# Kernel tuning notes

Measured on AMD Instinct MI355X. Metric: run time of the kernel, lower is better.

## Reference

```python
import jax, jax.numpy as jnp
import numpy as np

N = 100000      # nodes
E = 1600000     # edges (avg degree 16)
G = 64          # graphs in batch
IN_DIM, HID, C2, C3, HEADS, NCLS = 64, 128, 64, 32, 4, 5
EPS = 1e-5
NEG_SLOPE = 0.2


def setup_inputs() -> dict:
    key = jax.random.key(0)
    ks = jax.random.split(key, 32)

    def w(k, fan_in, shape):
        return jax.random.normal(k, shape, dtype=jnp.float32) * (1.0 / np.sqrt(fan_in))

    x = jax.random.normal(ks[0], (N, IN_DIM), dtype=jnp.float32)
    edge_index = jax.random.randint(ks[1], (2, E), 0, N)
    batch = jnp.sort(jax.random.randint(ks[2], (N,), 0, G))

    inp = {"x": x, "edge_index": edge_index, "batch": batch}
    # GCN layers (PyG GCNConv: weight then symmetric-normalized aggregation, bias after)
    inp.update(W1=w(ks[3], IN_DIM, (IN_DIM, HID)), b1=jnp.zeros((HID,), jnp.float32))
    inp.update(W2=w(ks[4], HID, (HID, C2)), b2=jnp.zeros((C2,), jnp.float32))
    inp.update(W3=w(ks[5], C2, (C2, C3)), b3=jnp.zeros((C3,), jnp.float32))
    # BatchNorm (inference: running stats)
    def bn_params(k, d):
        k1, k2, k3 = jax.random.split(k, 3)
        return (1.0 + 0.1 * jax.random.normal(k1, (d,), jnp.float32),
                0.1 * jax.random.normal(k2, (d,), jnp.float32),
                0.1 * jax.random.normal(k3, (d,), jnp.float32),
                jax.random.uniform(k, (d,), jnp.float32, 0.5, 1.5))
    inp["g1"], inp["be1"], inp["m1"], inp["v1"] = bn_params(ks[6], HID)
    inp["g2"], inp["be2"], inp["m2"], inp["v2"] = bn_params(ks[7], C2)
    inp["g3"], inp["be3"], inp["m3"], inp["v3"] = bn_params(ks[8], C3)
    # GAT (heads=4, out=32, concat=False -> mean over heads)
    inp["Wg"] = w(ks[9], C3, (C3, HEADS * C3))
    inp["ag_s"] = w(ks[10], C3, (HEADS, C3))
    inp["ag_d"] = w(ks[11], C3, (HEADS, C3))
    inp["bg"] = jnp.zeros((C3,), jnp.float32)
    # classifier MLP 32 -> 16 -> 5
    inp["Wc1"] = w(ks[12], C3, (C3, 16)); inp["bc1"] = jnp.zeros((16,), jnp.float32)
    inp["Wc2"] = w(ks[13], 16, (16, NCLS)); inp["bc2"] = jnp.zeros((NCLS,), jnp.float32)
    return inp


def _bn(h, g, be, m, v):
    return (h - m) * jax.lax.rsqrt(v + EPS) * g + be


def reference(x, edge_index, batch,
              W1, b1, g1, be1, m1, v1,
              W2, b2, g2, be2, m2, v2,
              W3, b3, g3, be3, m3, v3,
              Wg, ag_s, ag_d, bg,
              Wc1, bc1, Wc2, bc2):
    n = x.shape[0]
    loop = jnp.arange(n)
    src = jnp.concatenate([edge_index[0], loop])  # add self-loops (PyG default)
    dst = jnp.concatenate([edge_index[1], loop])

    # GCN symmetric normalization: deg from dst (col), norm = d^-1/2[src]*d^-1/2[dst]
    deg = jnp.zeros((n,), x.dtype).at[dst].add(1.0)
    dinv = jax.lax.rsqrt(deg)  # deg >= 1 due to self-loops
    norm = (dinv[src] * dinv[dst])[:, None]

    def gcn(h, W, b):
        h = h @ W
        return jax.ops.segment_sum(h[src] * norm, dst, num_segments=n) + b

    h = jax.nn.relu(_bn(gcn(x, W1, b1), g1, be1, m1, v1))
    h = jax.nn.relu(_bn(gcn(h, W2, b2), g2, be2, m2, v2))
    h = jax.nn.relu(_bn(gcn(h, W3, b3), g3, be3, m3, v3))

    # GAT: per-edge attention, segment softmax over incoming edges per dst
    hh = (h @ Wg).reshape(n, HEADS, C3)          # [N,H,D]
    a_s = jnp.einsum('nhd,hd->nh', hh, ag_s)     # [N,H]
    a_d = jnp.einsum('nhd,hd->nh', hh, ag_d)
    e = jax.nn.leaky_relu(a_s[src] + a_d[dst], NEG_SLOPE)  # [Eall,H]
    emax = jax.lax.stop_gradient(jax.ops.segment_max(e, dst, num_segments=n))
    ee = jnp.exp(e - emax[dst])
    den = jax.ops.segment_sum(ee, dst, num_segments=n)
    att = ee / den[dst]                          # [Eall,H]
    agg = jax.ops.segment_sum(att[:, :, None] * hh[src], dst, num_segments=n)
    h = jax.nn.relu(agg.mean(axis=1) + bg)       # concat=False -> mean heads

    # global mean pool over graphs
    cnt = jax.ops.segment_sum(jnp.ones((n,), h.dtype), batch, num_segments=G)
    pooled = jax.ops.segment_sum(h, batch, num_segments=G) / jnp.maximum(cnt, 1.0)[:, None]

    # classifier (dropout inactive in eval)
    out = jax.nn.relu(pooled @ Wc1 + bc1) @ Wc2 + bc2
    return out
```

## Files before the change

### kernel.cpp

```cpp
#include <hip/hip_runtime.h>

#define EPSN   1e-5f
#define NEGS   0.2f
#define NGRAPH 64
#define BSHIFT 9
#define NPBK   512
#define GCAP   96

__device__ __forceinline__ float lrelu(float e) { return e > 0.f ? e : NEGS * e; }

__global__ void k_bin_count(const int* __restrict__ ed, int* __restrict__ bsize,
                            int E, int NB) {
    __shared__ int lcnt[1024];
    for (int i = threadIdx.x; i < NB; i += 256) lcnt[i] = 0;
    __syncthreads();
    int chunk = (E + gridDim.x - 1) / gridDim.x;
    int lo = blockIdx.x * chunk;
    int hi = min(E, lo + chunk);
    for (int e = lo + threadIdx.x; e < hi; e += 256)
        atomicAdd(&lcnt[ed[e] >> BSHIFT], 1);
    __syncthreads();
    for (int b = threadIdx.x; b < NB; b += 256)
        if (lcnt[b]) atomicAdd(&bsize[b], lcnt[b]);
}
__global__ void k_bucket_scan(const int* __restrict__ bsize, int* __restrict__ bbase,
                              int* __restrict__ gcur, int NB) {
    int lane = threadIdx.x;
    if (lane >= 64) return;
    int carry = 0;
    int rounds = (NB + 63) / 64;
    for (int r = 0; r < rounds; ++r) {
        int idx = r * 64 + lane;
        int orig = (idx < NB) ? bsize[idx] : 0;
        int v = orig;
#pragma unroll
        for (int o = 1; o < 64; o <<= 1) {
            int t = __shfl_up(v, o, 64);
            if (lane >= o) v += t;
        }
        if (idx < NB) {
            int excl = carry + v - orig;
            bbase[idx] = excl;
            gcur[idx] = excl;
        }
        carry += __shfl(v, 63, 64);
    }
}
__global__ void k_bin_write(const int* __restrict__ es, const int* __restrict__ ed,
                            int* __restrict__ gcur, int2* __restrict__ binned,
                            int E, int NB) {
    __shared__ int lcnt[1024];
    __shared__ int lofs[1024];
    int chunk = (E + gridDim.x - 1) / gridDim.x;
    int lo = blockIdx.x * chunk;
    int hi = min(E, lo + chunk);
    for (int i = threadIdx.x; i < NB; i += 256) lcnt[i] = 0;
    __syncthreads();
    for (int e = lo + threadIdx.x; e < hi; e += 256)
        atomicAdd(&lcnt[ed[e] >> BSHIFT], 1);
    __syncthreads();
    for (int b = threadIdx.x; b < NB; b += 256) {
        int c = lcnt[b];
        lofs[b] = c ? atomicAdd(&gcur[b], c) : 0;
    }
    __syncthreads();
    for (int i = threadIdx.x; i < NB; i += 256) lcnt[i] = 0;
    __syncthreads();
    for (int e = lo + threadIdx.x; e < hi; e += 256) {
        int s = es[e], t = ed[e];
        int b = t >> BSHIFT;
        int pos = lofs[b] + atomicAdd(&lcnt[b], 1);
        binned[pos] = make_int2(s, t);
    }
}
__global__ void k_csr_build(const int2* __restrict__ binned, const int* __restrict__ bbase,
                            const int* __restrict__ bsize, int* __restrict__ rowptr,
                            int* __restrict__ deg, float* __restrict__ dinv,
                            int* __restrict__ csrc, int N) {
    __shared__ int cnt_l[NPBK];
    __shared__ int ofs_l[NPBK];
    int b = blockIdx.x;
    int base = bbase[b];
    int cnt = bsize[b];
    int nlo = b << BSHIFT;
    int nhi = min(N, nlo + NPBK);
    int nv = nhi - nlo;
    int csrbase = base + nlo;
    int tid = threadIdx.x;
    for (int i = tid; i < NPBK; i += 256) cnt_l[i] = (i < nv) ? 1 : 0;
    __syncthreads();
    for (int e = tid; e < cnt; e += 256) {
        int2 st = binned[base + e];
        atomicAdd(&cnt_l[st.y - nlo], 1);
    }
    __syncthreads();
    if (tid < 64) {
        int carry = 0;
#pragma unroll
        for (int r = 0; r < NPBK / 64; ++r) {
            int idx = r * 64 + tid;
            int orig = cnt_l[idx];
            int v = orig;
#pragma unroll
            for (int o = 1; o < 64; o <<= 1) {
                int t = __shfl_up(v, o, 64);
                if (tid >= o) v += t;
            }
            ofs_l[idx] = carry + v - orig;
            carry += __shfl(v, 63, 64);
        }
    }
    __syncthreads();
    for (int i = tid; i < nv; i += 256) {
        int node = nlo + i;
        int d = cnt_l[i];
        rowptr[node] = csrbase + ofs_l[i];
        deg[node] = d;
        dinv[node] = rsqrtf((float)d);
    }
    __syncthreads();
    for (int i = tid; i < NPBK; i += 256) cnt_l[i] = ofs_l[i];
    __syncthreads();
    for (int e = tid; e < cnt; e += 256) {
        int2 st = binned[base + e];
        int p = atomicAdd(&cnt_l[st.y - nlo], 1);
        csrc[csrbase + p] = st.x;
    }
    for (int i = tid; i < nv; i += 256) {
        int p = atomicAdd(&cnt_l[i], 1);
        csrc[csrbase + p] = nlo + i;
    }
}

template <int K, int M, int EPI>
__global__ void k_matmul4(const float* __restrict__ X, const float* __restrict__ W,
                          float* __restrict__ Y, int n,
                          const float* __restrict__ b, const float* __restrict__ g,
                          const float* __restrict__ be, const float* __restrict__ m,
                          const float* __restrict__ v, const float* __restrict__ dinv) {
    __shared__ float Wl[K * M];
    for (int i = threadIdx.x; i < K * M / 4; i += 256)
        ((float4*)Wl)[i] = ((const float4*)W)[i];
    __syncthreads();
    const int TPR = M / 4;
    const int RPB = 256 / TPR;
    const int c4  = (threadIdx.x % TPR) * 4;
    int row = blockIdx.x * RPB + threadIdx.x / TPR;
    if (row >= n) return;
    const float4* xr = (const float4*)(X + (long long)row * K);
    float4 acc = make_float4(0.f, 0.f, 0.f, 0.f);
#pragma unroll
    for (int k4 = 0; k4 < K / 4; ++k4) {
        float4 xv = xr[k4];
        const float* wp = &Wl[(k4 * 4) * M + c4];
        float4 w0 = *(const float4*)(wp);
        float4 w1 = *(const float4*)(wp + M);
        float4 w2 = *(const float4*)(wp + 2 * M);
        float4 w3 = *(const float4*)(wp + 3 * M);
        acc.x += xv.x * w0.x + xv.y * w1.x + xv.z * w2.x + xv.w * w3.x;
        acc.y += xv.x * w0.y + xv.y * w1.y + xv.z * w2.y + xv.w * w3.y;
        acc.z += xv.x * w0.z + xv.y * w1.z + xv.z * w2.z + xv.w * w3.z;
        acc.w += xv.x * w0.w + xv.y * w1.w + xv.z * w2.w + xv.w * w3.w;
    }
    if (EPI == 1) {
        float4 bb = *(const float4*)(b + c4);
        float4 mm = *(const float4*)(m + c4);
        float4 vv = *(const float4*)(v + c4);
        float4 gg = *(const float4*)(g + c4);
        float4 ee = *(const float4*)(be + c4);
        acc.x = fmaxf((acc.x + bb.x - mm.x) * rsqrtf(vv.x + EPSN) * gg.x + ee.x, 0.f);
        acc.y = fmaxf((acc.y + bb.y - mm.y) * rsqrtf(vv.y + EPSN) * gg.y + ee.y, 0.f);
        acc.z = fmaxf((acc.z + bb.z - mm.z) * rsqrtf(vv.z + EPSN) * gg.z + ee.z, 0.f);
        acc.w = fmaxf((acc.w + bb.w - mm.w) * rsqrtf(vv.w + EPSN) * gg.w + ee.w, 0.f);
    } else if (EPI == 2) {
        float din = dinv[row];
        acc.x *= din; acc.y *= din; acc.z *= din; acc.w *= din;
    }
    *(float4*)(Y + (long long)row * M + c4) = acc;
}

template <int M, int EPI, int PRE>
__global__ void k_agg4(const float* __restrict__ A, const int* __restrict__ rowptr,
                       const int* __restrict__ deg, const int* __restrict__ csrc,
                       const float* __restrict__ dinv,
                       const float* __restrict__ b, const float* __restrict__ g,
                       const float* __restrict__ be, const float* __restrict__ m,
                       const float* __restrict__ v,
                       float* __restrict__ B, int n) {
    const int LPE = M / 4;
    const int EPW = 64 / LPE;
    int node = blockIdx.x * 4 + (threadIdx.x >> 6);
    if (node >= n) return;
    int lane = threadIdx.x & 63;
    int eg = lane / LPE;
    int dl = lane % LPE;
    int beg = rowptr[node];
    int end = beg + deg[node];
    float4 acc = make_float4(0.f, 0.f, 0.f, 0.f);
    int i = beg + eg;
    for (; i + EPW < end; i += 2 * EPW) {
        int s0 = csrc[i];
        int s1 = csrc[i + EPW];
        float4 x0 = *(const float4*)(A + (long long)s0 * M + dl * 4);
        float4 x1 = *(const float4*)(A + (long long)s1 * M + dl * 4);
        if (PRE) {
            float w0 = dinv[s0], w1 = dinv[s1];
            x0.x *= w0; x0.y *= w0; x0.z *= w0; x0.w *= w0;
            x1.x *= w1; x1.y *= w1; x1.z *= w1; x1.w *= w1;
        }
        acc.x += x0.x + x1.x; acc.y += x0.y + x1.y;
        acc.z += x0.z + x1.z; acc.w += x0.w + x1.w;
    }
    if (i < end) {
        int s = csrc[i];
        float4 xv = *(const float4*)(A + (long long)s * M + dl * 4);
        if (PRE) {
            float w0 = dinv[s];
            xv.x *= w0; xv.y *= w0; xv.z *= w0; xv.w *= w0;
        }
        acc.x += xv.x; acc.y += xv.y; acc.z += xv.z; acc.w += xv.w;
    }
#pragma unroll
    for (int off = LPE; off < 64; off <<= 1) {
        acc.x += __shfl_xor(acc.x, off);
        acc.y += __shfl_xor(acc.y, off);
        acc.z += __shfl_xor(acc.z, off);
        acc.w += __shfl_xor(acc.w, off);
    }
    if (eg == 0) {
        float din = dinv[node];
        acc.x *= din; acc.y *= din; acc.z *= din; acc.w *= din;
        if (EPI == 1) {
            int d0 = dl * 4;
            float4 bb = *(const float4*)(b + d0);
            float4 mm = *(const float4*)(m + d0);
            float4 vv = *(const float4*)(v + d0);
            float4 gg = *(const float4*)(g + d0);
            float4 ee = *(const float4*)(be + d0);
            acc.x = fmaxf((acc.x + bb.x - mm.x) * rsqrtf(vv.x + EPSN) * gg.x + ee.x, 0.f);
            acc.y = fmaxf((acc.y + bb.y - mm.y) * rsqrtf(vv.y + EPSN) * gg.y + ee.y, 0.f);
            acc.z = fmaxf((acc.z + bb.z - mm.z) * rsqrtf(vv.z + EPSN) * gg.z + ee.z, 0.f);
            acc.w = fmaxf((acc.w + bb.w - mm.w) * rsqrtf(vv.w + EPSN) * gg.w + ee.w, 0.f);
        }
        *(float4*)(B + (long long)node * M + dl * 4) = acc;
    }
}

__global__ void k_wsd(const float* __restrict__ Wg, const float* __restrict__ ags,
                      const float* __restrict__ agd, float* __restrict__ wsd) {
    int j = threadIdx.x;
    if (j < 128) {
        int k = j >> 2, h = j & 3;
        float ss = 0.f, dd = 0.f;
        for (int d2 = 0; d2 < 32; ++d2) {
            float wv = Wg[k * 128 + h * 32 + d2];
            ss += wv * ags[h * 32 + d2];
            dd += wv * agd[h * 32 + d2];
        }
        wsd[j] = ss;
        wsd[128 + j] = dd;
    }
}

__global__ void k_agg_att(const float* __restrict__ A, const int* __restrict__ rowptr,
                          const int* __restrict__ deg, const int* __restrict__ csrc,
                          const float* __restrict__ dinv,
                          const float* __restrict__ b, const float* __restrict__ g,
                          const float* __restrict__ be, const float* __restrict__ m,
                          const float* __restrict__ v, const float* __restrict__ wsd,
                          float* __restrict__ H3, float* __restrict__ a_s,
                          float* __restrict__ a_d, int n) {
    __shared__ float Wl[256];
    for (int i = threadIdx.x; i < 256; i += 256) Wl[i] = wsd[i];
    __syncthreads();
    const int M = 32, LPE = 8, EPW = 8;
    int node = blockIdx.x * 4 + (threadIdx.x >> 6);
    if (node >= n) return;
    int lane = threadIdx.x & 63;
    int eg = lane >> 3;
    int dl = lane & 7;
    int beg = rowptr[node];
    int end = beg + deg[node];
    float4 acc = make_float4(0.f, 0.f, 0.f, 0.f);
    int i = beg + eg;
    for (; i + EPW < end; i += 2 * EPW) {
        int s0 = csrc[i];
        int s1 = csrc[i + EPW];
        float4 x0 = *(const float4*)(A + (long long)s0 * M + dl * 4);
        float4 x1 = *(const float4*)(A + (long long)s1 * M + dl * 4);
        acc.x += x0.x + x1.x; acc.y += x0.y + x1.y;
        acc.z += x0.z + x1.z; acc.w += x0.w + x1.w;
    }
    if (i < end) {
        int s = csrc[i];
        float4 xv = *(const float4*)(A + (long long)s * M + dl * 4);
        acc.x += xv.x; acc.y += xv.y; acc.z += xv.z; acc.w += xv.w;
    }
#pragma unroll
    for (int off = 8; off < 64; off <<= 1) {
        acc.x += __shfl_xor(acc.x, off);
        acc.y += __shfl_xor(acc.y, off);
        acc.z += __shfl_xor(acc.z, off);
        acc.w += __shfl_xor(acc.w, off);
    }
    float din = dinv[node];
    int d0 = dl * 4;
    float4 bb = *(const float4*)(b + d0);
    float4 mm = *(const float4*)(m + d0);
    float4 vv = *(const float4*)(v + d0);
    float4 gg = *(const float4*)(g + d0);
    float4 ee = *(const float4*)(be + d0);
    float4 hv;
    hv.x = fmaxf((acc.x * din + bb.x - mm.x) * rsqrtf(vv.x + EPSN) * gg.x + ee.x, 0.f);
    hv.y = fmaxf((acc.y * din + bb.y - mm.y) * rsqrtf(vv.y + EPSN) * gg.y + ee.y, 0.f);
    hv.z = fmaxf((acc.z * din + bb.z - mm.z) * rsqrtf(vv.z + EPSN) * gg.z + ee.z, 0.f);
    hv.w = fmaxf((acc.w * din + bb.w - mm.w) * rsqrtf(vv.w + EPSN) * gg.w + ee.w, 0.f);
    if (eg == 0)
        *(float4*)(H3 + (long long)node * M + d0) = hv;
    int h = lane & 3, sel = (lane >> 2) & 1;
    const float* wp = &Wl[sel * 128];
    float o = 0.f;
#pragma unroll
    for (int src = 0; src < 8; ++src) {
        float bx = __shfl(hv.x, src);
        float by = __shfl(hv.y, src);
        float bz = __shfl(hv.z, src);
        float bw = __shfl(hv.w, src);
        int k0 = src * 4;
        o += bx * wp[k0 * 4 + h] + by * wp[(k0 + 1) * 4 + h] +
             bz * wp[(k0 + 2) * 4 + h] + bw * wp[(k0 + 3) * 4 + h];
    }
    if (lane < 4) a_s[node * 4 + h] = o;
    else if (lane < 8) a_d[node * 4 + h] = o;
}

__global__ void k_gat4(const float* __restrict__ H3, const float* __restrict__ a_s,
                       const float* __restrict__ a_d, const int* __restrict__ rowptr,
                       const int* __restrict__ deg, const int* __restrict__ csrc,
                       const float* __restrict__ Wg, const float* __restrict__ bg,
                       float* __restrict__ H4, int n) {
    __shared__ float sc[4][GCAP * 4];
    __shared__ int   srcb[4][GCAP];
    __shared__ float wb[4][128];
    int w = threadIdx.x >> 6;
    int node = blockIdx.x * 4 + w;
    if (node >= n) return;
    int lane = threadIdx.x & 63;
    int beg = rowptr[node];
    int cnt = deg[node];
    bool fits = (cnt <= GCAP);
    float4 ad4 = ((const float4*)a_d)[node];
    float m0 = -1e30f, m1 = -1e30f, m2 = -1e30f, m3 = -1e30f;
    if (fits) {
        for (int e = lane; e < cnt; e += 64) {
            int s = csrc[beg + e];
            srcb[w][e] = s;
            float4 as = ((const float4*)a_s)[s];
            float e0 = lrelu(as.x + ad4.x);
            float e1 = lrelu(as.y + ad4.y);
            float e2 = lrelu(as.z + ad4.z);
            float e3 = lrelu(as.w + ad4.w);
            *(float4*)&sc[w][e * 4] = make_float4(e0, e1, e2, e3);
            m0 = fmaxf(m0, e0); m1 = fmaxf(m1, e1);
            m2 = fmaxf(m2, e2); m3 = fmaxf(m3, e3);
        }
    } else {
        for (int e = lane; e < cnt; e += 64) {
            int s = csrc[beg + e];
            float4 as = ((const float4*)a_s)[s];
            m0 = fmaxf(m0, lrelu(as.x + ad4.x));
            m1 = fmaxf(m1, lrelu(as.y + ad4.y));
            m2 = fmaxf(m2, lrelu(as.z + ad4.z));
            m3 = fmaxf(m3, lrelu(as.w + ad4.w));
        }
    }
#pragma unroll
    for (int o = 1; o < 64; o <<= 1) {
        m0 = fmaxf(m0, __shfl_xor(m0, o));
        m1 = fmaxf(m1, __shfl_xor(m1, o));
        m2 = fmaxf(m2, __shfl_xor(m2, o));
        m3 = fmaxf(m3, __shfl_xor(m3, o));
    }
    float s0 = 0.f, s1 = 0.f, s2 = 0.f, s3 = 0.f;
    if (fits) {
        for (int e = lane; e < cnt; e += 64) {
            float4 sv = *(float4*)&sc[w][e * 4];
            float p0 = __expf(sv.x - m0);
            float p1 = __expf(sv.y - m1);
            float p2 = __expf(sv.z - m2);
            float p3 = __expf(sv.w - m3);
            *(float4*)&sc[w][e * 4] = make_float4(p0, p1, p2, p3);
            s0 += p0; s1 += p1; s2 += p2; s3 += p3;
        }
    } else {
        for (int e = lane; e < cnt; e += 64) {
            int s = csrc[beg + e];
            float4 as = ((const float4*)a_s)[s];
            s0 += __expf(lrelu(as.x + ad4.x) - m0);
            s1 += __expf(lrelu(as.y + ad4.y) - m1);
            s2 += __expf(lrelu(as.z + ad4.z) - m2);
            s3 += __expf(lrelu(as.w + ad4.w) - m3);
        }
    }
#pragma unroll
    for (int o = 1; o < 64; o <<= 1) {
        s0 += __shfl_xor(s0, o);
        s1 += __shfl_xor(s1, o);
        s2 += __shfl_xor(s2, o);
        s3 += __shfl_xor(s3, o);
    }
    float inv0 = 0.25f / s0, inv1 = 0.25f / s1, inv2 = 0.25f / s2, inv3 = 0.25f / s3;
    int d = lane & 31;
    int h0 = lane >> 5;
    float invA = (h0 == 0) ? inv0 : inv1;
    float invB = (h0 == 0) ? inv2 : inv3;
    float a0 = 0.f, a1 = 0.f;
    if (fits) {
        int i = 0;
        for (; i + 4 <= cnt; i += 4) {
            int sA = srcb[w][i],     sB = srcb[w][i + 1];
            int sC = srcb[w][i + 2], sD = srcb[w][i + 3];
            float x0 = H3[(long long)sA * 32 + d];
            float x1 = H3[(long long)sB * 32 + d];
            float x2 = H3[(long long)sC * 32 + d];
            float x3 = H3[(long long)sD * 32 + d];
            float wA0 = sc[w][i * 4 + h0],       wA1 = sc[w][i * 4 + h0 + 2];
            float wB0 = sc[w][(i + 1) * 4 + h0], wB1 = sc[w][(i + 1) * 4 + h0 + 2];
            float wC0 = sc[w][(i + 2) * 4 + h0], wC1 = sc[w][(i + 2) * 4 + h0 + 2];
            float wD0 = sc[w][(i + 3) * 4 + h0], wD1 = sc[w][(i + 3) * 4 + h0 + 2];
            a0 += wA0 * x0 + wB0 * x1 + wC0 * x2 + wD0 * x3;
            a1 += wA1 * x0 + wB1 * x1 + wC1 * x2 + wD1 * x3;
        }
        for (; i < cnt; ++i) {
            int s = srcb[w][i];
            float x = H3[(long long)s * 32 + d];
            a0 += sc[w][i * 4 + h0] * x;
            a1 += sc[w][i * 4 + h0 + 2] * x;
        }
        a0 *= invA; a1 *= invB;
    } else {
        float mA = (h0 == 0) ? m0 : m1;
        float mB = (h0 == 0) ? m2 : m3;
        float adA = (h0 == 0) ? ad4.x : ad4.y;
        float adB = (h0 == 0) ? ad4.z : ad4.w;
        for (int i = 0; i < cnt; ++i) {
            int s = csrc[beg + i];
            float4 as = ((const float4*)a_s)[s];
            float eA = (h0 == 0) ? (as.x + adA) : (as.y + adA);
            float eB = (h0 == 0) ? (as.z + adB) : (as.w + adB);
            float x = H3[(long long)s * 32 + d];
            a0 += __expf(lrelu(eA) - mA) * x;
            a1 += __expf(lrelu(eB) - mB) * x;
        }
        a0 *= invA; a1 *= invB;
    }
    wb[w][lane] = a0;
    wb[w][64 + lane] = a1;
    int half = h0 * 64;
    float o = 0.f;
#pragma unroll
    for (int j = 0; j < 64; ++j) {
        int jj = half + j;
        o += wb[w][jj] * Wg[(jj & 31) * 128 + (jj >> 5) * 32 + d];
    }
    o += __shfl_xor(o, 32);
    if (lane < 32)
        H4[(long long)node * 32 + d] = fmaxf(o + bg[d], 0.f);
}

__global__ void k_pool_init(float* __restrict__ pooled, float* __restrict__ cnt) {
    int i = blockIdx.x * blockDim.x + threadIdx.x;
    if (i < NGRAPH * 32) pooled[i] = 0.f;
    if (i < NGRAPH) cnt[i] = 0.f;
}
__global__ void k_pool2(const float* __restrict__ h, const int* __restrict__ batch,
                        float* __restrict__ pooled, float* __restrict__ cnt, int n) {
    __shared__ float lp[NGRAPH * 32];
    __shared__ float lc[NGRAPH];
    int tid = threadIdx.x;
    for (int i = tid; i < NGRAPH * 32; i += 256) lp[i] = 0.f;
    for (int i = tid; i < NGRAPH; i += 256) lc[i] = 0.f;
    __syncthreads();
    int per = (n + gridDim.x - 1) / gridDim.x;
    int lo = blockIdx.x * per;
    int hi = min(n, lo + per);
    for (long long i = (long long)lo * 32 + tid; i < (long long)hi * 32; i += 256) {
        int ni = (int)(i >> 5), dd = (int)(i & 31);
        int b = batch[ni];
        atomicAdd(&lp[b * 32 + dd], h[i]);
        if (dd == 0) atomicAdd(&lc[b], 1.f);
    }
    __syncthreads();
    for (int i = tid; i < NGRAPH * 32; i += 256)
        if (lp[i] != 0.f) atomicAdd(&pooled[i], lp[i]);
    for (int i = tid; i < NGRAPH; i += 256)
        if (lc[i] != 0.f) atomicAdd(&cnt[i], lc[i]);
}

__global__ void k_classifier(const float* __restrict__ pooled, const float* __restrict__ cnt,
                             const float* __restrict__ Wc1, const float* __restrict__ bc1,
                             const float* __restrict__ Wc2, const float* __restrict__ bc2,
                             float* __restrict__ out) {
    __shared__ float pl[NGRAPH * 32];
    __shared__ float t1[NGRAPH * 16];
    int tid = threadIdx.x;
    for (int i = tid; i < NGRAPH * 32; i += blockDim.x) {
        int g = i >> 5;
        pl[i] = pooled[i] / fmaxf(cnt[g], 1.f);
    }
    __syncthreads();
    for (int i = tid; i < NGRAPH * 16; i += blockDim.x) {
        int g = i >> 4, c = i & 15;
        float acc = bc1[c];
#pragma unroll
        for (int d = 0; d < 32; ++d) acc += pl[g * 32 + d] * Wc1[d * 16 + c];
        t1[i] = fmaxf(acc, 0.f);
    }
    __syncthreads();
    for (int i = tid; i < NGRAPH * 5; i += blockDim.x) {
        int g = i / 5, c = i % 5;
        float acc = bc2[c];
#pragma unroll
        for (int k = 0; k < 16; ++k) acc += t1[g * 16 + k] * Wc2[k * 5 + c];
        out[i] = acc;
    }
}

static inline dim3 gsz(long long work, int block = 256) {
    long long g = (work + block - 1) / block;
    if (g > 262144) g = 262144;
    if (g < 1) g = 1;
    return dim3((unsigned)g);
}

extern "C" void kernel_launch(void* const* d_in, const int* in_sizes, int n_in,
                              void* d_out, int out_size, void* d_ws, size_t ws_size,
                              hipStream_t stream) {
    const float* x     = (const float*)d_in[0];
    const int*   ei    = (const int*)d_in[1];
    const int*   batch = (const int*)d_in[2];
    const float* W1 = (const float*)d_in[3];  const float* b1 = (const float*)d_in[4];
    const float* W2 = (const float*)d_in[5];  const float* b2 = (const float*)d_in[6];
    const float* W3 = (const float*)d_in[7];  const float* b3 = (const float*)d_in[8];
    const float* g1 = (const float*)d_in[9];  const float* be1 = (const float*)d_in[10];
    const float* m1 = (const float*)d_in[11]; const float* v1  = (const float*)d_in[12];
    const float* g2 = (const float*)d_in[13]; const float* be2 = (const float*)d_in[14];
    const float* m2 = (const float*)d_in[15]; const float* v2  = (const float*)d_in[16];
    const float* g3 = (const float*)d_in[17]; const float* be3 = (const float*)d_in[18];
    const float* m3 = (const float*)d_in[19]; const float* v3  = (const float*)d_in[20];
    const float* Wg  = (const float*)d_in[21];
    const float* ags = (const float*)d_in[22];
    const float* agd = (const float*)d_in[23];
    const float* bg  = (const float*)d_in[24];
    const float* Wc1 = (const float*)d_in[25]; const float* bc1 = (const float*)d_in[26];
    const float* Wc2 = (const float*)d_in[27]; const float* bc2 = (const float*)d_in[28];
    float* out = (float*)d_out;

    const int N = in_sizes[0] / 64;
    const int E = in_sizes[1] / 2;
    const int* esrc = ei;
    const int* edst = ei + E;
    const int NB = (N + NPBK - 1) >> BSHIFT;

    size_t off = 0;
    auto take = [&](size_t bytes) -> void* {
        void* p = (char*)d_ws + off;
        off += bytes;
        off = (off + 255) & ~(size_t)255;
        return p;
    };
    int*   deg    = (int*)take((size_t)N * 4);
    float* dinv   = (float*)take((size_t)N * 4);
    int*   rowptr = (int*)take((size_t)N * 4);
    int*   bsize  = (int*)take((size_t)1024 * 4);
    int*   bbase  = (int*)take((size_t)1024 * 4);
    int*   gcur   = (int*)take((size_t)1024 * 4);
    float* wsd    = (float*)take((size_t)256 * 4);
    int*   csrc   = (int*)take((size_t)(E + N) * 4);
    float* bufA   = (float*)take((size_t)N * 64 * 4);
    float* bufB   = (float*)take((size_t)N * 64 * 4);
    float* bufC   = (float*)take((size_t)N * 128 * 4);
    float* a_s    = (float*)take((size_t)N * 4 * 4);
    float* a_d    = (float*)take((size_t)N * 4 * 4);
    float* pooled = (float*)take((size_t)NGRAPH * 32 * 4);
    float* cnt    = (float*)take((size_t)NGRAPH * 4);
    int2*  binned = (int2*)bufC;
    (void)ws_size; (void)n_in; (void)out_size;

    const dim3 B256(256);
    const float* nil = nullptr;

    hipMemsetAsync(bsize, 0, (size_t)NB * 4, stream);
    hipLaunchKernelGGL(k_bin_count, dim3(512), B256, 0, stream, edst, bsize, E, NB);
    hipLaunchKernelGGL(k_bucket_scan, dim3(1), dim3(64), 0, stream, bsize, bbase, gcur, NB);
    hipLaunchKernelGGL(k_bin_write, dim3(512), B256, 0, stream, esrc, edst, gcur, binned, E, NB);
    hipLaunchKernelGGL(k_csr_build, dim3(NB), B256, 0, stream,
                       binned, bbase, bsize, rowptr, deg, dinv, csrc, N);
    hipLaunchKernelGGL(k_wsd, dim3(1), dim3(128), 0, stream, Wg, ags, agd, wsd);

    hipLaunchKernelGGL((k_agg4<64, 0, 1>), dim3((N + 3) / 4), B256, 0, stream,
                       x, rowptr, deg, csrc, dinv, nil, nil, nil, nil, nil, bufB, N);
    hipLaunchKernelGGL((k_matmul4<64, 128, 1>), dim3((N + 7) / 8), B256, 0, stream,
                       bufB, W1, bufC, N, b1, g1, be1, m1, v1, nil);
    hipLaunchKernelGGL((k_matmul4<128, 64, 2>), dim3((N + 15) / 16), B256, 0, stream,
                       bufC, W2, bufA, N, nil, nil, nil, nil, nil, dinv);
    hipLaunchKernelGGL((k_agg4<64, 1, 0>), dim3((N + 3) / 4), B256, 0, stream,
                       bufA, rowptr, deg, csrc, dinv, b2, g2, be2, m2, v2, bufB, N);
    hipLaunchKernelGGL((k_matmul4<64, 32, 2>), dim3((N + 31) / 32), B256, 0, stream,
                       bufB, W3, bufA, N, nil, nil, nil, nil, nil, dinv);
    hipLaunchKernelGGL(k_agg_att, dim3((N + 3) / 4), B256, 0, stream,
                       bufA, rowptr, deg, csrc, dinv, b3, g3, be3, m3, v3,
                       wsd, bufB, a_s, a_d, N);

    hipLaunchKernelGGL(k_gat4, dim3((N + 3) / 4), B256, 0, stream,
                       bufB, a_s, a_d, rowptr, deg, csrc, Wg, bg, bufA, N);

    hipLaunchKernelGGL(k_pool_init, dim3(9), B256, 0, stream, pooled, cnt);
    hipLaunchKernelGGL(k_pool2, dim3(128), B256, 0, stream, bufA, batch, pooled, cnt, N);
    hipLaunchKernelGGL(k_classifier, dim3(1), B256, 0, stream, pooled, cnt, Wc1, bc1, Wc2, bc2, out);
}
```

Before: 655.1 us.

## Store gathered node features in fp16 to halve neighbor gather bandwidth

Node feature buffers read by the edge aggregations (input x, the GCN layer-2 and layer-3 projected features, and the GAT input H3) are now stored as fp16. They are converted back to fp32 for accumulation. A new kernel pre-scales x by dinv and converts it to fp16, replacing the in-loop dinv multiply. The GAT aggregation is restructured so each lane loads half2 features and accumulates all four heads at once. This cuts memory traffic of the gather-bound aggregations, at the cost of reduced precision and an extra conversion pass.

Result: faster. 633.1 us (-3.4%).

```diff
diff --git a/kernel.cpp b/kernel.cpp
--- a/kernel.cpp
+++ b/kernel.cpp
@@ -6,6 +6,11 @@
 #define BSHIFT 9
 #define NPBK   512
 #define GCAP   96
+
+typedef _Float16 half_t;
+typedef _Float16 halfv8 __attribute__((ext_vector_type(8)));
+typedef _Float16 halfv4 __attribute__((ext_vector_type(4)));
+typedef _Float16 halfv2 __attribute__((ext_vector_type(2)));
 
 __device__ __forceinline__ float lrelu(float e) { return e > 0.f ? e : NEGS * e; }
 
@@ -132,12 +137,29 @@
     }
 }
 
-template <int K, int M, int EPI>
+__global__ void k_cvt_xh(const float* __restrict__ x, const float* __restrict__ dinv,
+                         half_t* __restrict__ xh, int n) {
+    int total = n * 8;
+    for (int q = blockIdx.x * blockDim.x + threadIdx.x; q < total;
+         q += gridDim.x * blockDim.x) {
+        float din = dinv[q >> 3];
+        float4 a = ((const float4*)x)[q * 2];
+        float4 b = ((const float4*)x)[q * 2 + 1];
+        halfv8 h;
+        h[0] = (half_t)(a.x * din); h[1] = (half_t)(a.y * din);
+        h[2] = (half_t)(a.z * din); h[3] = (half_t)(a.w * din);
+        h[4] = (half_t)(b.x * din); h[5] = (half_t)(b.y * din);
+        h[6] = (half_t)(b.z * din); h[7] = (half_t)(b.w * din);
+        ((halfv8*)xh)[q] = h;
+    }
+}
+
+template <int K, int M>
 __global__ void k_matmul4(const float* __restrict__ X, const float* __restrict__ W,
                           float* __restrict__ Y, int n,
                           const float* __restrict__ b, const float* __restrict__ g,
                           const float* __restrict__ be, const float* __restrict__ m,
-                          const float* __restrict__ v, const float* __restrict__ dinv) {
+                          const float* __restrict__ v) {
     __shared__ float Wl[K * M];
     for (int i = threadIdx.x; i < K * M / 4; i += 256)
         ((float4*)Wl)[i] = ((const float4*)W)[i];
@@ -162,32 +184,61 @@
         acc.z += xv.x * w0.z + xv.y * w1.z + xv.z * w2.z + xv.w * w3.z;
         acc.w += xv.x * w0.w + xv.y * w1.w + xv.z * w2.w + xv.w * w3.w;
     }
-    if (EPI == 1) {
-        float4 bb = *(const float4*)(b + c4);
-        float4 mm = *(const float4*)(m + c4);
-        float4 vv = *(const float4*)(v + c4);
-        float4 gg = *(const float4*)(g + c4);
-        float4 ee = *(const float4*)(be + c4);
-        acc.x = fmaxf((acc.x + bb.x - mm.x) * rsqrtf(vv.x + EPSN) * gg.x + ee.x, 0.f);
-        acc.y = fmaxf((acc.y + bb.y - mm.y) * rsqrtf(vv.y + EPSN) * gg.y + ee.y, 0.f);
-        acc.z = fmaxf((acc.z + bb.z - mm.z) * rsqrtf(vv.z + EPSN) * gg.z + ee.z, 0.f);
-        acc.w = fmaxf((acc.w + bb.w - mm.w) * rsqrtf(vv.w + EPSN) * gg.w + ee.w, 0.f);
-    } else if (EPI == 2) {
-        float din = dinv[row];
-        acc.x *= din; acc.y *= din; acc.z *= din; acc.w *= din;
-    }
+    float4 bb = *(const float4*)(b + c4);
+    float4 mm = *(const float4*)(m + c4);
+    float4 vv = *(const float4*)(v + c4);
+    float4 gg = *(const float4*)(g + c4);
+    float4 ee = *(const float4*)(be + c4);
+    acc.x = fmaxf((acc.x + bb.x - mm.x) * rsqrtf(vv.x + EPSN) * gg.x + ee.x, 0.f);
+    acc.y = fmaxf((acc.y + bb.y - mm.y) * rsqrtf(vv.y + EPSN) * gg.y + ee.y, 0.f);
+    acc.z = fmaxf((acc.z + bb.z - mm.z) * rsqrtf(vv.z + EPSN) * gg.z + ee.z, 0.f);
+    acc.w = fmaxf((acc.w + bb.w - mm.w) * rsqrtf(vv.w + EPSN) * gg.w + ee.w, 0.f);
     *(float4*)(Y + (long long)row * M + c4) = acc;
 }
 
-template <int M, int EPI, int PRE>
-__global__ void k_agg4(const float* __restrict__ A, const int* __restrict__ rowptr,
-                       const int* __restrict__ deg, const int* __restrict__ csrc,
-                       const float* __restrict__ dinv,
-                       const float* __restrict__ b, const float* __restrict__ g,
-                       const float* __restrict__ be, const float* __restrict__ m,
-                       const float* __restrict__ v,
-                       float* __restrict__ B, int n) {
-    const int LPE = M / 4;
+template <int K, int M>
+__global__ void k_matmul4h(const float* __restrict__ X, const float* __restrict__ W,
+                           half_t* __restrict__ Y, int n, const float* __restrict__ dinv) {
+    __shared__ float Wl[K * M];
+    for (int i = threadIdx.x; i < K * M / 4; i += 256)
+        ((float4*)Wl)[i] = ((const float4*)W)[i];
+    __syncthreads();
+    const int TPR = M / 4;
+    const int RPB = 256 / TPR;
+    const int c4  = (threadIdx.x % TPR) * 4;
+    int row = blockIdx.x * RPB + threadIdx.x / TPR;
+    if (row >= n) return;
+    const float4* xr = (const float4*)(X + (long long)row * K);
+    float4 acc = make_float4(0.f, 0.f, 0.f, 0.f);
+#pragma unroll
+    for (int k4 = 0; k4 < K / 4; ++k4) {
+        float4 xv = xr[k4];
+        const float* wp = &Wl[(k4 * 4) * M + c4];
+        float4 w0 = *(const float4*)(wp);
+        float4 w1 = *(const float4*)(wp + M);
+        float4 w2 = *(const float4*)(wp + 2 * M);
+        float4 w3 = *(const float4*)(wp + 3 * M);
+        acc.x += xv.x * w0.x + xv.y * w1.x + xv.z * w2.x + xv.w * w3.x;
+        acc.y += xv.x * w0.y + xv.y * w1.y + xv.z * w2.y + xv.w * w3.y;
+        acc.z += xv.x * w0.z + xv.y * w1.z + xv.z * w2.z + xv.w * w3.z;
+        acc.w += xv.x * w0.w + xv.y * w1.w + xv.z * w2.w + xv.w * w3.w;
+    }
+    float din = dinv[row];
+    halfv4 hv;
+    hv[0] = (half_t)(acc.x * din); hv[1] = (half_t)(acc.y * din);
+    hv[2] = (half_t)(acc.z * din); hv[3] = (half_t)(acc.w * din);
+    *(halfv4*)(Y + (long long)row * M + c4) = hv;
+}
+
+template <int M, int EPI>
+__global__ void k_agg4h(const half_t* __restrict__ A, const int* __restrict__ rowptr,
+                        const int* __restrict__ deg, const int* __restrict__ csrc,
+                        const float* __restrict__ dinv,
+                        const float* __restrict__ b, const float* __restrict__ g,
+                        const float* __restrict__ be, const float* __restrict__ m,
+                        const float* __restrict__ v,
+                        float* __restrict__ B, int n) {
+    const int LPE = M / 8;
     const int EPW = 64 / LPE;
     int node = blockIdx.x * 4 + (threadIdx.x >> 6);
     if (node >= n) return;
@@ -196,53 +247,46 @@
     int dl = lane % LPE;
     int beg = rowptr[node];
     int end = beg + deg[node];
-    float4 acc = make_float4(0.f, 0.f, 0.f, 0.f);
+    float acc[8];
+#pragma unroll
+    for (int j = 0; j < 8; ++j) acc[j] = 0.f;
     int i = beg + eg;
     for (; i + EPW < end; i += 2 * EPW) {
         int s0 = csrc[i];
         int s1 = csrc[i + EPW];
-        float4 x0 = *(const float4*)(A + (long long)s0 * M + dl * 4);
-        float4 x1 = *(const float4*)(A + (long long)s1 * M + dl * 4);
-        if (PRE) {
-            float w0 = dinv[s0], w1 = dinv[s1];
-            x0.x *= w0; x0.y *= w0; x0.z *= w0; x0.w *= w0;
-            x1.x *= w1; x1.y *= w1; x1.z *= w1; x1.w *= w1;
-        }
-        acc.x += x0.x + x1.x; acc.y += x0.y + x1.y;
-        acc.z += x0.z + x1.z; acc.w += x0.w + x1.w;
+        halfv8 x0 = *(const halfv8*)(A + (long long)s0 * M + dl * 8);
+        halfv8 x1 = *(const halfv8*)(A + (long long)s1 * M + dl * 8);
+#pragma unroll
+        for (int j = 0; j < 8; ++j) acc[j] += (float)x0[j] + (float)x1[j];
     }
     if (i < end) {
         int s = csrc[i];
-        float4 xv = *(const float4*)(A + (long long)s * M + dl * 4);
-        if (PRE) {
-            float w0 = dinv[s];
-            xv.x *= w0; xv.y *= w0; xv.z *= w0; xv.w *= w0;
-        }
-        acc.x += xv.x; acc.y += xv.y; acc.z += xv.z; acc.w += xv.w;
+        halfv8 xv = *(const halfv8*)(A + (long long)s * M + dl * 8);
+#pragma unroll
+        for (int j = 0; j < 8; ++j) acc[j] += (float)xv[j];
     }
 #pragma unroll
     for (int off = LPE; off < 64; off <<= 1) {
-        acc.x += __shfl_xor(acc.x, off);
-        acc.y += __shfl_xor(acc.y, off);
-        acc.z += __shfl_xor(acc.z, off);
-        acc.w += __shfl_xor(acc.w, off);
+#pragma unroll
+        for (int j = 0; j < 8; ++j) acc[j] += __shfl_xor(acc[j], off);
     }
     if (eg == 0) {
         float din = dinv[node];
-        acc.x *= din; acc.y *= din; acc.z *= din; acc.w *= din;
+        int d0 = dl * 8;
+        float o[8];
+#pragma unroll
+        for (int j = 0; j < 8; ++j) o[j] = acc[j] * din;
         if (EPI == 1) {
-            int d0 = dl * 4;
-            float4 bb = *(const float4*)(b + d0);
-            float4 mm = *(const float4*)(m + d0);
-            float4 vv = *(const float4*)(v + d0);
-            float4 gg = *(const float4*)(g + d0);
-            float4 ee = *(const float4*)(be + d0);
-            acc.x = fmaxf((acc.x + bb.x - mm.x) * rsqrtf(vv.x + EPSN) * gg.x + ee.x, 0.f);
-            acc.y = fmaxf((acc.y + bb.y - mm.y) * rsqrtf(vv.y + EPSN) * gg.y + ee.y, 0.f);
-            acc.z = fmaxf((acc.z + bb.z - mm.z) * rsqrtf(vv.z + EPSN) * gg.z + ee.z, 0.f);
-            acc.w = fmaxf((acc.w + bb.w - mm.w) * rsqrtf(vv.w + EPSN) * gg.w + ee.w, 0.f);
-        }
-        *(float4*)(B + (long long)node * M + dl * 4) = acc;
+#pragma unroll
+            for (int j = 0; j < 8; ++j) {
+                int d = d0 + j;
+                o[j] = fmaxf((o[j] + b[d] - m[d]) * rsqrtf(v[d] + EPSN) * g[d] + be[d], 0.f);
+            }
+        }
+        float4 lo = make_float4(o[0], o[1], o[2], o[3]);
+        float4 hi = make_float4(o[4], o[5], o[6], o[7]);
+        *(float4*)(B + (long long)node * M + d0) = lo;
+        *(float4*)(B + (long long)node * M + d0 + 4) = hi;
     }
 }
 
@@ -262,79 +306,78 @@
     }
 }
 
-__global__ void k_agg_att(const float* __restrict__ A, const int* __restrict__ rowptr,
+__global__ void k_agg_att(const half_t* __restrict__ A, const int* __restrict__ rowptr,
                           const int* __restrict__ deg, const int* __restrict__ csrc,
                           const float* __restrict__ dinv,
                           const float* __restrict__ b, const float* __restrict__ g,
                           const float* __restrict__ be, const float* __restrict__ m,
                           const float* __restrict__ v, const float* __restrict__ wsd,
-                          float* __restrict__ H3, float* __restrict__ a_s,
+                          half_t* __restrict__ H3h, float* __restrict__ a_s,
                           float* __restrict__ a_d, int n) {
     __shared__ float Wl[256];
     for (int i = threadIdx.x; i < 256; i += 256) Wl[i] = wsd[i];
     __syncthreads();
-    const int M = 32, LPE = 8, EPW = 8;
+    const int M = 32, LPE = 4, EPW = 16;
     int node = blockIdx.x * 4 + (threadIdx.x >> 6);
     if (node >= n) return;
     int lane = threadIdx.x & 63;
-    int eg = lane >> 3;
-    int dl = lane & 7;
+    int eg = lane >> 2;
+    int dl = lane & 3;
     int beg = rowptr[node];
     int end = beg + deg[node];
-    float4 acc = make_float4(0.f, 0.f, 0.f, 0.f);
+    float acc[8];
+#pragma unroll
+    for (int j = 0; j < 8; ++j) acc[j] = 0.f;
     int i = beg + eg;
     for (; i + EPW < end; i += 2 * EPW) {
         int s0 = csrc[i];
         int s1 = csrc[i + EPW];
-        float4 x0 = *(const float4*)(A + (long long)s0 * M + dl * 4);
-        float4 x1 = *(const float4*)(A + (long long)s1 * M + dl * 4);
-        acc.x += x0.x + x1.x; acc.y += x0.y + x1.y;
-        acc.z += x0.z + x1.z; acc.w += x0.w + x1.w;
+        halfv8 x0 = *(const halfv8*)(A + (long long)s0 * M + dl * 8);
+        halfv8 x1 = *(const halfv8*)(A + (long long)s1 * M + dl * 8);
+#pragma unroll
+        for (int j = 0; j < 8; ++j) acc[j] += (float)x0[j] + (float)x1[j];
     }
     if (i < end) {
         int s = csrc[i];
-        float4 xv = *(const float4*)(A + (long long)s * M + dl * 4);
-        acc.x += xv.x; acc.y += xv.y; acc.z += xv.z; acc.w += xv.w;
-    }
-#pragma unroll
-    for (int off = 8; off < 64; off <<= 1) {
-        acc.x += __shfl_xor(acc.x, off);
-        acc.y += __shfl_xor(acc.y, off);
-        acc.z += __shfl_xor(acc.z, off);
-        acc.w += __shfl_xor(acc.w, off);
+        halfv8 xv = *(const halfv8*)(A + (long long)s * M + dl * 8);
+#pragma unroll
+        for (int j = 0; j < 8; ++j) acc[j] += (float)xv[j];
+    }
+#pragma unroll
+    for (int off = 4; off < 64; off <<= 1) {
+#pragma unroll
+        for (int j = 0; j < 8; ++j) acc[j] += __shfl_xor(acc[j], off);
     }
     float din = dinv[node];
-    int d0 = dl * 4;
-    float4 bb = *(const float4*)(b + d0);
-    float4 mm = *(const float4*)(m + d0);
-    float4 vv = *(const float4*)(v + d0);
-    float4 gg = *(const float4*)(g + d0);
-    float4 ee = *(const float4*)(be + d0);
-    float4 hv;
-    hv.x = fmaxf((acc.x * din + bb.x - mm.x) * rsqrtf(vv.x + EPSN) * gg.x + ee.x, 0.f);
-    hv.y = fmaxf((acc.y * din + bb.y - mm.y) * rsqrtf(vv.y + EPSN) * gg.y + ee.y, 0.f);
-    hv.z = fmaxf((acc.z * din + bb.z - mm.z) * rsqrtf(vv.z + EPSN) * gg.z + ee.z, 0.f);
-    hv.w = fmaxf((acc.w * din + bb.w - mm.w) * rsqrtf(vv.w + EPSN) * gg.w + ee.w, 0.f);
-    if (eg == 0)
-        *(float4*)(H3 + (long long)node * M + d0) = hv;
+    int d0 = dl * 8;
+    float hv[8];
+#pragma unroll
+    for (int j = 0; j < 8; ++j) {
+        int d = d0 + j;
+        hv[j] = fmaxf((acc[j] * din + b[d] - m[d]) * rsqrtf(v[d] + EPSN) * g[d] + be[d], 0.f);
+    }
+    if (eg == 0) {
+        halfv8 hw;
+#pragma unroll
+        for (int j = 0; j < 8; ++j) hw[j] = (half_t)hv[j];
+        *(halfv8*)(H3h + (long long)node * M + d0) = hw;
+    }
     int h = lane & 3, sel = (lane >> 2) & 1;
     const float* wp = &Wl[sel * 128];
     float o = 0.f;
 #pragma unroll
-    for (int src = 0; src < 8; ++src) {
-        float bx = __shfl(hv.x, src);
-        float by = __shfl(hv.y, src);
-        float bz = __shfl(hv.z, src);
-        float bw = __shfl(hv.w, src);
-        int k0 = src * 4;
-        o += bx * wp[k0 * 4 + h] + by * wp[(k0 + 1) * 4 + h] +
-             bz * wp[(k0 + 2) * 4 + h] + bw * wp[(k0 + 3) * 4 + h];
+    for (int src = 0; src < 4; ++src) {
+#pragma unroll
+        for (int j = 0; j < 8; ++j) {
+            float xv = __shfl(hv[j], src);
+            o += xv * wp[(src * 8 + j) * 4 + h];
+        }
     }
     if (lane < 4) a_s[node * 4 + h] = o;
     else if (lane < 8) a_d[node * 4 + h] = o;
 }
 
-__global__ void k_gat4(const float* __restrict__ H3, const float* __restrict__ a_s,
+__global__ void k_gat4(const half_t* __restrict__ H3h, const float* __restrict__ a_s,
                        const float* __restrict__ a_d, const int* __restrict__ rowptr,
                        const int* __restrict__ deg, const int* __restrict__ csrc,
                        const float* __restrict__ Wg, const float* __restrict__ bg,
@@ -410,57 +453,73 @@
         s3 += __shfl_xor(s3, o);
     }
     float inv0 = 0.25f / s0, inv1 = 0.25f / s1, inv2 = 0.25f / s2, inv3 = 0.25f / s3;
+    int q = lane >> 4;
+    int k = lane & 15;
+    float acc[8];
+#pragma unroll
+    for (int j = 0; j < 8; ++j) acc[j] = 0.f;
+    if (fits) {
+        int i = q;
+        for (; i + 4 < cnt; i += 8) {
+            int sA = srcb[w][i];
+            int sB = srcb[w][i + 4];
+            halfv2 xA = *(const halfv2*)(H3h + (long long)sA * 32 + 2 * k);
+            halfv2 xB = *(const halfv2*)(H3h + (long long)sB * 32 + 2 * k);
+            float4 wA = *(float4*)&sc[w][i * 4];
+            float4 wB = *(float4*)&sc[w][(i + 4) * 4];
+            float a0 = (float)xA[0], a1 = (float)xA[1];
+            float b0 = (float)xB[0], b1 = (float)xB[1];
+            acc[0] += wA.x * a0 + wB.x * b0; acc[1] += wA.x * a1 + wB.x * b1;
+            acc[2] += wA.y * a0 + wB.y * b0; acc[3] += wA.y * a1 + wB.y * b1;
+            acc[4] += wA.z * a0 + wB.z * b0; acc[5] += wA.z * a1 + wB.z * b1;
+            acc[6] += wA.w * a0 + wB.w * b0; acc[7] += wA.w * a1 + wB.w * b1;
+        }
+        if (i < cnt) {
+            int s = srcb[w][i];
+            halfv2 xv = *(const halfv2*)(H3h + (long long)s * 32 + 2 * k);
+            float4 wv = *(float4*)&sc[w][i * 4];
+            float x0 = (float)xv[0], x1 = (float)xv[1];
+            acc[0] += wv.x * x0; acc[1] += wv.x * x1;
+            acc[2] += wv.y * x0; acc[3] += wv.y * x1;
+            acc[4] += wv.z * x0; acc[5] += wv.z * x1;
+            acc[6] += wv.w * x0; acc[7] += wv.w * x1;
+        }
+    } else {
+        for (int i = q; i < cnt; i += 4) {
+            int s = csrc[beg + i];
+            float4 as = ((const float4*)a_s)[s];
+            float p0 = __expf(lrelu(as.x + ad4.x) - m0);
+            float p1 = __expf(lrelu(as.y + ad4.y) - m1);
+            float p2 = __expf(lrelu(as.z + ad4.z) - m2);
+            float p3 = __expf(lrelu(as.w + ad4.w) - m3);
+            halfv2 xv = *(const halfv2*)(H3h + (long long)s * 32 + 2 * k);
+            float x0 = (float)xv[0], x1 = (float)xv[1];
+            acc[0] += p0 * x0; acc[1] += p0 * x1;
+            acc[2] += p1 * x0; acc[3] += p1 * x1;
+            acc[4] += p2 * x0; acc[5] += p2 * x1;
+            acc[6] += p3 * x0; acc[7] += p3 * x1;
+        }
+    }
+#pragma unroll
+    for (int o = 16; o < 64; o <<= 1) {
+#pragma unroll
+        for (int j = 0; j < 8; ++j) acc[j] += __shfl_xor(acc[j], o);
+    }
+    if (q == 0) {
+        float invh[4] = {inv0, inv1, inv2, inv3};
+#pragma unroll
+        for (int h = 0; h < 4; ++h) {
+            wb[w][h * 32 + 2 * k]     = acc[h * 2]     * invh[h];
+            wb[w][h * 32 + 2 * k + 1] = acc[h * 2 + 1] * invh[h];
+        }
+    }
     int d = lane & 31;
     int h0 = lane >> 5;
-    float invA = (h0 == 0) ? inv0 : inv1;
-    float invB = (h0 == 0) ? inv2 : inv3;
-    float a0 = 0.f, a1 = 0.f;
-    if (fits) {
-        int i = 0;
-        for (; i + 4 <= cnt; i += 4) {
-            int sA = srcb[w][i],     sB = srcb[w][i + 1];
-            int sC = srcb[w][i + 2], sD = srcb[w][i + 3];
-            float x0 = H3[(long long)sA * 32 + d];
-            float x1 = H3[(long long)sB * 32 + d];
-            float x2 = H3[(long long)sC * 32 + d];
-            float x3 = H3[(long long)sD * 32 + d];
-            float wA0 = sc[w][i * 4 + h0],       wA1 = sc[w][i * 4 + h0 + 2];
-            float wB0 = sc[w][(i + 1) * 4 + h0], wB1 = sc[w][(i + 1) * 4 + h0 + 2];
-            float wC0 = sc[w][(i + 2) * 4 + h0], wC1 = sc[w][(i + 2) * 4 + h0 + 2];
-            float wD0 = sc[w][(i + 3) * 4 + h0], wD1 = sc[w][(i + 3) * 4 + h0 + 2];
-            a0 += wA0 * x0 + wB0 * x1 + wC0 * x2 + wD0 * x3;
-            a1 += wA1 * x0 + wB1 * x1 + wC1 * x2 + wD1 * x3;
-        }
-        for (; i < cnt; ++i) {
-            int s = srcb[w][i];
-            float x = H3[(long long)s * 32 + d];
-            a0 += sc[w][i * 4 + h0] * x;
-            a1 += sc[w][i * 4 + h0 + 2] * x;
-        }
-        a0 *= invA; a1 *= invB;
-    } else {
-        float mA = (h0 == 0) ? m0 : m1;
-        float mB = (h0 == 0) ? m2 : m3;
-        float adA = (h0 == 0) ? ad4.x : ad4.y;
-        float adB = (h0 == 0) ? ad4.z : ad4.w;
-        for (int i = 0; i < cnt; ++i) {
-            int s = csrc[beg + i];
-            float4 as = ((const float4*)a_s)[s];
-            float eA = (h0 == 0) ? (as.x + adA) : (as.y + adA);
-            float eB = (h0 == 0) ? (as.z + adB) : (as.w + adB);
-            float x = H3[(long long)s * 32 + d];
-            a0 += __expf(lrelu(eA) - mA) * x;
-            a1 += __expf(lrelu(eB) - mB) * x;
-        }
-        a0 *= invA; a1 *= invB;
-    }
-    wb[w][lane] = a0;
-    wb[w][64 + lane] = a1;
-    int half = h0 * 64;
+    int half_ = h0 * 64;
     float o = 0.f;
 #pragma unroll
     for (int j = 0; j < 64; ++j) {
-        int jj = half + j;
+        int jj = half_ + j;
         o += wb[w][jj] * Wg[(jj & 31) * 128 + (jj >> 5) * 32 + d];
     }
     o += __shfl_xor(o, 32);
@@ -569,26 +628,27 @@
         off = (off + 255) & ~(size_t)255;
         return p;
     };
-    int*   deg    = (int*)take((size_t)N * 4);
-    float* dinv   = (float*)take((size_t)N * 4);
-    int*   rowptr = (int*)take((size_t)N * 4);
-    int*   bsize  = (int*)take((size_t)1024 * 4);
-    int*   bbase  = (int*)take((size_t)1024 * 4);
-    int*   gcur   = (int*)take((size_t)1024 * 4);
-    float* wsd    = (float*)take((size_t)256 * 4);
-    int*   csrc   = (int*)take((size_t)(E + N) * 4);
-    float* bufA   = (float*)take((size_t)N * 64 * 4);
-    float* bufB   = (float*)take((size_t)N * 64 * 4);
-    float* bufC   = (float*)take((size_t)N * 128 * 4);
-    float* a_s    = (float*)take((size_t)N * 4 * 4);
-    float* a_d    = (float*)take((size_t)N * 4 * 4);
-    float* pooled = (float*)take((size_t)NGRAPH * 32 * 4);
-    float* cnt    = (float*)take((size_t)NGRAPH * 4);
-    int2*  binned = (int2*)bufC;
+    int*    deg    = (int*)take((size_t)N * 4);
+    float*  dinv   = (float*)take((size_t)N * 4);
+    int*    rowptr = (int*)take((size_t)N * 4);
+    int*    bsize  = (int*)take((size_t)1024 * 4);
+    int*    bbase  = (int*)take((size_t)1024 * 4);
+    int*    gcur   = (int*)take((size_t)1024 * 4);
+    float*  wsd    = (float*)take((size_t)256 * 4);
+    int*    csrc   = (int*)take((size_t)(E + N) * 4);
+    half_t* bufAh  = (half_t*)take((size_t)N * 64 * 2);
+    float*  bufB   = (float*)take((size_t)N * 64 * 4);
+    float*  bufC   = (float*)take((size_t)N * 128 * 4);
+    half_t* h3h    = (half_t*)take((size_t)N * 32 * 2);
+    float*  a_s    = (float*)take((size_t)N * 4 * 4);
+    float*  a_d    = (float*)take((size_t)N * 4 * 4);
+    float*  pooled = (float*)take((size_t)NGRAPH * 32 * 4);
+    float*  cnt    = (float*)take((size_t)NGRAPH * 4);
+    int2*   binned = (int2*)bufC;
+    float*  H4     = (float*)bufAh;
     (void)ws_size; (void)n_in; (void)out_size;
 
     const dim3 B256(256);
-    const float* nil = nullptr;
 
     hipMemsetAsync(bsize, 0, (size_t)NB * 4, stream);
     hipLaunchKernelGGL(k_bin_count, dim3(512), B256, 0, stream, edst, bsize, E, NB);
@@ -598,24 +658,26 @@
                        binned, bbase, bsize, rowptr, deg, dinv, csrc, N);
     hipLaunchKernelGGL(k_wsd, dim3(1), dim3(128), 0, stream, Wg, ags, agd, wsd);
 
-    hipLaunchKernelGGL((k_agg4<64, 0, 1>), dim3((N + 3) / 4), B256, 0, stream,
-                       x, rowptr, deg, csrc, dinv, nil, nil, nil, nil, nil, bufB, N);
-    hipLaunchKernelGGL((k_matmul4<64, 128, 1>), dim3((N + 7) / 8), B256, 0, stream,
-                       bufB, W1, bufC, N, b1, g1, be1, m1, v1, nil);
-    hipLaunchKernelGGL((k_matmul4<128, 64, 2>), dim3((N + 15) / 16), B256, 0, stream,
-                       bufC, W2, bufA, N, nil, nil, nil, nil, nil, dinv);
-    hipLaunchKernelGGL((k_agg4<64, 1, 0>), dim3((N + 3) / 4), B256, 0, stream,
-                       bufA, rowptr, deg, csrc, dinv, b2, g2, be2, m2, v2, bufB, N);
-    hipLaunchKernelGGL((k_matmul4<64, 32, 2>), dim3((N + 31) / 32), B256, 0, stream,
-                       bufB, W3, bufA, N, nil, nil, nil, nil, nil, dinv);
+    hipLaunchKernelGGL(k_cvt_xh, gsz((long long)N * 8), B256, 0, stream, x, dinv, bufAh, N);
+    hipLaunchKernelGGL((k_agg4h<64, 0>), dim3((N + 3) / 4), B256, 0, stream,
+                       bufAh, rowptr, deg, csrc, dinv,
+                       nullptr, nullptr, nullptr, nullptr, nullptr, bufB, N);
+    hipLaunchKernelGGL((k_matmul4<64, 128>), dim3((N + 7) / 8), B256, 0, stream,
+                       bufB, W1, bufC, N, b1, g1, be1, m1, v1);
+    hipLaunchKernelGGL((k_matmul4h<128, 64>), dim3((N + 15) / 16), B256, 0, stream,
+                       bufC, W2, bufAh, N, dinv);
+    hipLaunchKernelGGL((k_agg4h<64, 1>), dim3((N + 3) / 4), B256, 0, stream,
+                       bufAh, rowptr, deg, csrc, dinv, b2, g2, be2, m2, v2, bufB, N);
+    hipLaunchKernelGGL((k_matmul4h<64, 32>), dim3((N + 31) / 32), B256, 0, stream,
+                       bufB, W3, bufAh, N, dinv);
     hipLaunchKernelGGL(k_agg_att, dim3((N + 3) / 4), B256, 0, stream,
-                       bufA, rowptr, deg, csrc, dinv, b3, g3, be3, m3, v3,
-                       wsd, bufB, a_s, a_d, N);
+                       bufAh, rowptr, deg, csrc, dinv, b3, g3, be3, m3, v3,
+                       wsd, h3h, a_s, a_d, N);
 
     hipLaunchKernelGGL(k_gat4, dim3((N + 3) / 4), B256, 0, stream,
-                       bufB, a_s, a_d, rowptr, deg, csrc, Wg, bg, bufA, N);
+                       h3h, a_s, a_d, rowptr, deg, csrc, Wg, bg, H4, N);
 
     hipLaunchKernelGGL(k_pool_init, dim3(9), B256, 0, stream, pooled, cnt);
-    hipLaunchKernelGGL(k_pool2, dim3(128), B256, 0, stream, bufA, batch, pooled, cnt, N);
+    hipLaunchKernelGGL(k_pool2, dim3(128), B256, 0, stream, H4, batch, pooled, cnt, N);
     hipLaunchKernelGGL(k_classifier, dim3(1), B256, 0, stream, pooled, cnt, Wc1, bc1, Wc2, bc2, out);
 }
```
